# Kernel tuning notes

Hardware: AMD Instinct MI355X
Metric: run time of the kernel (lower is better)

## Reference

```python
import jax, jax.numpy as jnp
import numpy as np
import math

N, NP, D, H, W, HEADS = 4, 1024, 256, 64, 64, 8
DH = D // HEADS


def _norm_coords(height, width):
    # (height*width, 2) with (x, y) in [0, 1], row-major flatten (y outer, x inner)
    y = jnp.linspace(0.0, 1.0, height)
    x = jnp.linspace(0.0, 1.0, width)
    yg, xg = jnp.meshgrid(y, x, indexing='ij')
    return jnp.stack([xg.reshape(-1), yg.reshape(-1)], axis=-1)


def _pos_enc(coords, dim):
    # coords: (P, 2) -> (P, dim); even slots sin(x*div), odd slots cos(y*div)
    div = jnp.exp(jnp.arange(0, dim, 2, dtype=coords.dtype) * (-math.log(10000.0) / dim))
    s = jnp.sin(coords[:, 0:1] * div)  # (P, dim/2)
    c = jnp.cos(coords[:, 1:2] * div)  # (P, dim/2)
    return jnp.stack([s, c], axis=-1).reshape(coords.shape[0], dim)


def setup_inputs() -> dict:
    key = jax.random.key(0)
    ks = jax.random.split(key, 10)
    sc = 1.0 / math.sqrt(D)
    return {
        "local_feat": jax.random.normal(ks[0], (N, NP, D), jnp.float32),
        "global_feat": jax.random.normal(ks[1], (N, D, H, W), jnp.float32),
        "Wq": jax.random.normal(ks[2], (D, D), jnp.float32) * sc,
        "bq": jax.random.normal(ks[3], (D,), jnp.float32) * sc,
        "Wk": jax.random.normal(ks[4], (D, D), jnp.float32) * sc,
        "bk": jax.random.normal(ks[5], (D,), jnp.float32) * sc,
        "Wv": jax.random.normal(ks[6], (D, D), jnp.float32) * sc,
        "bv": jax.random.normal(ks[7], (D,), jnp.float32) * sc,
        "Wo": jax.random.normal(ks[8], (D, D), jnp.float32) * sc,
        "bo": jax.random.normal(ks[9], (D,), jnp.float32) * sc,
    }


def reference(local_feat, global_feat, Wq, bq, Wk, bk, Wv, bv, Wo, bo):
    n, N_p, d = local_feat.shape
    _, _, h, w = global_feat.shape
    hw = h * w
    P = int(math.sqrt(N_p))

    gf = jnp.transpose(global_feat.reshape(n, d, hw), (0, 2, 1))  # (n, HW, d)

    lf = local_feat + _pos_enc(_norm_coords(P, P), d)[None]       # (n, N_p, d)
    gf = gf + _pos_enc(_norm_coords(h, w), d)[None]               # (n, HW, d)

    q = (lf @ Wq.T + bq).reshape(n, N_p, HEADS, DH)
    k = (gf @ Wk.T + bk).reshape(n, hw, HEADS, DH)
    v = (gf @ Wv.T + bv).reshape(n, hw, HEADS, DH)

    scores = jnp.einsum('bqhd,bkhd->bhqk', q, k) / math.sqrt(DH)  # (n, H, N_p, HW)
    attn = jax.nn.softmax(scores, axis=-1)
    out = jnp.einsum('bhqk,bkhd->bqhd', attn, v).reshape(n, N_p, d)

    return (lf + out) @ Wo.T + bo
```

## Files before the change

### kernel.cpp

```cpp
#include <hip/hip_runtime.h>
#include <hip/hip_bf16.h>
#include <math.h>

#define NB    4
#define NPTS  1024
#define DD    256
#define HWW   4096
#define NHEAD 8
#define DHD   32
#define VTROW 4128

typedef short s8v  __attribute__((ext_vector_type(8)));
typedef float f4v  __attribute__((ext_vector_type(4)));
typedef unsigned int u2v __attribute__((ext_vector_type(2)));
typedef unsigned int u4v __attribute__((ext_vector_type(4)));

#define MFMA_BF16 __builtin_amdgcn_mfma_f32_16x16x32_bf16

#define PE_FACT (-9.210340371976184f / 256.0f)
#define QSCALE 0.2550348637f

#if defined(__has_builtin)
#if __has_builtin(__builtin_amdgcn_permlane16_swap) && __has_builtin(__builtin_amdgcn_permlane32_swap)
#define HAVE_PLSWAP 1
#endif
#endif

__device__ __forceinline__ unsigned packbf(float hi, float lo) {
    return __builtin_amdgcn_perm(__float_as_uint(hi), __float_as_uint(lo), 0x07060302u);
}

__device__ __forceinline__ void swap2(unsigned a, unsigned b, unsigned& x, unsigned& y) {
#ifdef HAVE_PLSWAP
    u2v r1 = __builtin_amdgcn_permlane32_swap(a, b, false, false);
    u2v r2 = __builtin_amdgcn_permlane16_swap(r1.x, r1.y, false, false);
    x = r2.x; y = r2.y;
#else
    int l = threadIdx.x & 63;
    int i0 = ((((l >> 4) & 1) << 5) | (l & 15)) << 2;
    unsigned pa = (unsigned)__builtin_amdgcn_ds_bpermute(i0, (int)a);
    unsigned pb = (unsigned)__builtin_amdgcn_ds_bpermute(i0, (int)b);
    x = (l < 32) ? pa : pb;
    unsigned qa = (unsigned)__builtin_amdgcn_ds_bpermute(i0 + 64, (int)a);
    unsigned qb = (unsigned)__builtin_amdgcn_ds_bpermute(i0 + 64, (int)b);
    y = (l < 32) ? qa : qb;
#endif
}

__global__ __launch_bounds__(256) void prep_local(const float* __restrict__ lf,
                                                  __hip_bfloat16* __restrict__ lf_pe_b) {
    int idx = blockIdx.x * 256 + threadIdx.x;
    int c = idx & 255;
    int p = (idx >> 8) & 1023;
    float div = __expf((float)(c & ~1) * PE_FACT);
    float pe;
    if (c & 1) {
        float y = (float)(p >> 5) * (1.0f / 31.0f);
        pe = __cosf(y * div);
    } else {
        float x = (float)(p & 31) * (1.0f / 31.0f);
        pe = __sinf(x * div);
    }
    lf_pe_b[idx] = __float2bfloat16(lf[idx] + pe);
}

__global__ __launch_bounds__(1024) void prep_global(const float* __restrict__ gfeat,
                                                    __hip_bfloat16* __restrict__ gf_pe_b) {
    __shared__ float tile[32][33];
    int n  = blockIdx.z;
    int p0 = blockIdx.x * 32;
    int c0 = blockIdx.y * 32;
    int tx = threadIdx.x, ty = threadIdx.y;
    tile[ty][tx] = gfeat[((size_t)n * DD + (c0 + ty)) * HWW + p0 + tx];
    __syncthreads();
    int p = p0 + ty, c = c0 + tx;
    float div = __expf((float)(c & ~1) * PE_FACT);
    float pe;
    if (c & 1) {
        float y = (float)(p >> 6) * (1.0f / 63.0f);
        pe = __cosf(y * div);
    } else {
        float x = (float)(p & 63) * (1.0f / 63.0f);
        pe = __sinf(x * div);
    }
    gf_pe_b[((size_t)n * HWW + p) * DD + c] = __float2bfloat16(tile[tx][ty] + pe);
}

__global__ __launch_bounds__(256) void w2b(const float* __restrict__ wq, const float* __restrict__ wk,
                                           const float* __restrict__ wv, const float* __restrict__ wo,
                                           __hip_bfloat16* __restrict__ out) {
    int idx = blockIdx.x * 256 + threadIdx.x;
    int m = idx >> 16, r = idx & 65535;
    const float* src = (m == 0) ? wq : (m == 1) ? wk : (m == 2) ? wv : wo;
    out[idx] = __float2bfloat16(src[r]);
}

template <int MODE>
__global__ __launch_bounds__(256) void gemm256(const __hip_bfloat16* __restrict__ A,
                                               const __hip_bfloat16* __restrict__ Wb,
                                               const float* __restrict__ bias,
                                               void* __restrict__ outp) {
    int wave = threadIdx.x >> 6;
    int lane = threadIdx.x & 63;
    int quad = lane >> 4, c16 = lane & 15;
    int m0 = blockIdx.x * 64 + wave * 16;
    int c0 = blockIdx.y * 64;
    const short* ap  = (const short*)A + (m0 + c16) * DD + quad * 8;
    const short* wp  = (const short*)Wb + (c0 + c16) * DD + quad * 8;

    f4v acc0 = {0.f, 0.f, 0.f, 0.f}, acc1 = acc0, acc2 = acc0, acc3 = acc0;

    s8v a  = *(const s8v*)(ap);
    s8v b0 = *(const s8v*)(wp);
    s8v b1 = *(const s8v*)(wp + 16 * DD);
    s8v b2 = *(const s8v*)(wp + 32 * DD);
    s8v b3 = *(const s8v*)(wp + 48 * DD);
#pragma unroll
    for (int ks = 0; ks < 8; ++ks) {
        s8v an, bn0, bn1, bn2, bn3;
        if (ks < 7) {
            int o = (ks + 1) * 32;
            an  = *(const s8v*)(ap + o);
            bn0 = *(const s8v*)(wp + o);
            bn1 = *(const s8v*)(wp + o + 16 * DD);
            bn2 = *(const s8v*)(wp + o + 32 * DD);
            bn3 = *(const s8v*)(wp + o + 48 * DD);
        }
        acc0 = MFMA_BF16(a, b0, acc0, 0, 0, 0);
        acc1 = MFMA_BF16(a, b1, acc1, 0, 0, 0);
        acc2 = MFMA_BF16(a, b2, acc2, 0, 0, 0);
        acc3 = MFMA_BF16(a, b3, acc3, 0, 0, 0);
        if (ks < 7) { a = an; b0 = bn0; b1 = bn1; b2 = bn2; b3 = bn3; }
    }
#pragma unroll
    for (int t = 0; t < 4; ++t) {
        f4v acc = (t == 0) ? acc0 : (t == 1) ? acc1 : (t == 2) ? acc2 : acc3;
        int col = c0 + t * 16 + c16;
        float bv = bias[col];
#pragma unroll
        for (int r = 0; r < 4; ++r) {
            int row = m0 + quad * 4 + r;
            float v = acc[r] + bv;
            if (MODE == 0) {
                int n = row >> 10, p = row & 1023, h = col >> 5, dh = col & 31;
                ((__hip_bfloat16*)outp)[(((size_t)(n * NHEAD + h) << 10) + p) * DHD + dh] =
                    __float2bfloat16(v * QSCALE);
            } else {
                ((float*)outp)[(size_t)row * DD + col] = v;
            }
        }
    }
}

__global__ __launch_bounds__(256) void gemmKV(const __hip_bfloat16* __restrict__ A,
                                              const __hip_bfloat16* __restrict__ Wk,
                                              const __hip_bfloat16* __restrict__ Wv,
                                              const float* __restrict__ bk,
                                              const float* __restrict__ bv,
                                              __hip_bfloat16* __restrict__ Kb,
                                              __hip_bfloat16* __restrict__ Vtb) {
    __shared__ __align__(16) unsigned stv[64][36];

    int tid = threadIdx.x;
    int wave = tid >> 6;
    int lane = tid & 63;
    int quad = lane >> 4, c16 = lane & 15;
    int m0 = blockIdx.x * 64 + wave * 16;
    int c0 = blockIdx.y * 64;
    const short* ap  = (const short*)A + (m0 + c16) * DD + quad * 8;
    const short* wkp = (const short*)Wk + (c0 + c16) * DD + quad * 8;
    const short* wvp = (const short*)Wv + (c0 + c16) * DD + quad * 8;

    f4v ak0 = {0.f,0.f,0.f,0.f}, ak1 = ak0, ak2 = ak0, ak3 = ak0;
    f4v av0 = ak0, av1 = ak0, av2 = ak0, av3 = ak0;

    s8v a  = *(const s8v*)(ap);
    s8v k0 = *(const s8v*)(wkp);
    s8v k1 = *(const s8v*)(wkp + 16 * DD);
    s8v k2 = *(const s8v*)(wkp + 32 * DD);
    s8v k3 = *(const s8v*)(wkp + 48 * DD);
    s8v v0 = *(const s8v*)(wvp);
    s8v v1 = *(const s8v*)(wvp + 16 * DD);
    s8v v2 = *(const s8v*)(wvp + 32 * DD);
    s8v v3 = *(const s8v*)(wvp + 48 * DD);
#pragma unroll
    for (int ks = 0; ks < 8; ++ks) {
        s8v an, kn0, kn1, kn2, kn3, vn0, vn1, vn2, vn3;
        if (ks < 7) {
            int o = (ks + 1) * 32;
            an  = *(const s8v*)(ap + o);
            kn0 = *(const s8v*)(wkp + o);
            kn1 = *(const s8v*)(wkp + o + 16 * DD);
            kn2 = *(const s8v*)(wkp + o + 32 * DD);
            kn3 = *(const s8v*)(wkp + o + 48 * DD);
            vn0 = *(const s8v*)(wvp + o);
            vn1 = *(const s8v*)(wvp + o + 16 * DD);
            vn2 = *(const s8v*)(wvp + o + 32 * DD);
            vn3 = *(const s8v*)(wvp + o + 48 * DD);
        }
        ak0 = MFMA_BF16(a, k0, ak0, 0, 0, 0);
        ak1 = MFMA_BF16(a, k1, ak1, 0, 0, 0);
        ak2 = MFMA_BF16(a, k2, ak2, 0, 0, 0);
        ak3 = MFMA_BF16(a, k3, ak3, 0, 0, 0);
        av0 = MFMA_BF16(a, v0, av0, 0, 0, 0);
        av1 = MFMA_BF16(a, v1, av1, 0, 0, 0);
        av2 = MFMA_BF16(a, v2, av2, 0, 0, 0);
        av3 = MFMA_BF16(a, v3, av3, 0, 0, 0);
        if (ks < 7) {
            a = an; k0 = kn0; k1 = kn1; k2 = kn2; k3 = kn3;
            v0 = vn0; v1 = vn1; v2 = vn2; v3 = vn3;
        }
    }
    int nblk = (blockIdx.x * 64) >> 12;
    int kb   = (blockIdx.x * 64) & 4095;
#pragma unroll
    for (int t = 0; t < 4; ++t) {
        f4v accK = (t == 0) ? ak0 : (t == 1) ? ak1 : (t == 2) ? ak2 : ak3;
        f4v accV = (t == 0) ? av0 : (t == 1) ? av1 : (t == 2) ? av2 : av3;
        int col = c0 + t * 16 + c16;
        float bkv = bk[col], bvv = bv[col];
        int h = col >> 5, dh = col & 31;
#pragma unroll
        for (int r = 0; r < 4; ++r) {
            int row = m0 + quad * 4 + r;
            int p = row & 4095;
            Kb[(((size_t)(nblk * NHEAD + h) << 12) + p) * DHD + dh] = __float2bfloat16(accK[r] + bkv);
        }
#pragma unroll
        for (int rp = 0; rp < 2; ++rp) {
            __hip_bfloat16 lo = __float2bfloat16(accV[2 * rp] + bvv);
            __hip_bfloat16 hi = __float2bfloat16(accV[2 * rp + 1] + bvv);
            unsigned dw = (unsigned)*(unsigned short*)&lo | ((unsigned)*(unsigned short*)&hi << 16);
            stv[t * 16 + c16][wave * 8 + quad * 2 + rp] = dw;
        }
    }
    __syncthreads();
    int col = tid >> 2;
    int kd  = (tid & 3) * 8;
    u4v w0 = *(const u4v*)&stv[col][kd];
    u4v w1 = *(const u4v*)&stv[col][kd + 4];
    int gh  = (c0 + col) >> 5, gdh = (c0 + col) & 31;
    short* vp = (short*)Vtb + ((size_t)(nblk * NHEAD + gh) * DHD + gdh) * VTROW + kb + kd * 2;
    *(u4v*)(vp)     = w0;
    *(u4v*)(vp + 8) = w1;
}

template <int NC>
__global__ __launch_bounds__(256) void attn(const __hip_bfloat16* __restrict__ Q,
                                            const __hip_bfloat16* __restrict__ Kg,
                                            const __hip_bfloat16* __restrict__ Vt,
                                            __hip_bfloat16* __restrict__ Opart,
                                            float* __restrict__ lpart) {
    constexpr int CK = HWW / NC;
    constexpr int NSTEP = CK / 32;

    int tid = threadIdx.x;
    int wave = tid >> 6, lane = tid & 63;
    int quad = lane >> 4, c16 = lane & 15;

    int id = blockIdx.x;
    int xcd = id & 7;
    int s = id >> 3;
    int qtile = s & 3;
    int gidx = ((s >> 2) << 3) | xcd;
    int bh = gidx & 31;
    int chunk = gidx >> 5;

    int q0 = qtile * 256 + wave * 64;

    const short* Qs = (const short*)Q + (size_t)bh * NPTS * DHD;
    const short* Ks = (const short*)Kg + ((size_t)bh * HWW + (size_t)chunk * CK) * DHD;
    const short* Vs = (const short*)Vt + (size_t)bh * DHD * VTROW + (size_t)chunk * CK;

    s8v aq[4];
#pragma unroll
    for (int g = 0; g < 4; ++g)
        aq[g] = *(const s8v*)(Qs + (q0 + g * 16 + c16) * DHD + quad * 8);

    const f4v zf = {0.f, 0.f, 0.f, 0.f};
    f4v o[4][2];
#pragma unroll
    for (int g = 0; g < 4; ++g) { o[g][0] = zf; o[g][1] = zf; }
    float lsum[4] = {0.f, 0.f, 0.f, 0.f};

    const short* kbase  = Ks + c16 * DHD + quad * 8;
    const short* v0base = Vs + c16 * VTROW + quad * 8;
    const short* v1base = Vs + (16 + c16) * VTROW + quad * 8;

    s8v kfA = *(const s8v*)(kbase);
    s8v kfB = *(const s8v*)(kbase + 16 * DHD);
    s8v vfA = *(const s8v*)(v0base);
    s8v vfB = *(const s8v*)(v1base);

    for (int st = 0; st < NSTEP; ++st) {
        bool more = (st + 1) < NSTEP;
        s8v nkA, nkB, nvA, nvB;
        if (more) {
            int ko = (st + 1) * 32;
            nkA = *(const s8v*)(kbase + ko * DHD);
            nkB = *(const s8v*)(kbase + ko * DHD + 16 * DHD);
            nvA = *(const s8v*)(v0base + ko);
            nvB = *(const s8v*)(v1base + ko);
        }
#pragma unroll
        for (int g = 0; g < 4; ++g) {
            f4v sA = MFMA_BF16(kfA, aq[g], zf, 0, 0, 0);
            f4v sB = MFMA_BF16(kfB, aq[g], zf, 0, 0, 0);
            float pA0 = __builtin_amdgcn_exp2f(sA[0]);
            float pA1 = __builtin_amdgcn_exp2f(sA[1]);
            float pA2 = __builtin_amdgcn_exp2f(sA[2]);
            float pA3 = __builtin_amdgcn_exp2f(sA[3]);
            float pB0 = __builtin_amdgcn_exp2f(sB[0]);
            float pB1 = __builtin_amdgcn_exp2f(sB[1]);
            float pB2 = __builtin_amdgcn_exp2f(sB[2]);
            float pB3 = __builtin_amdgcn_exp2f(sB[3]);
            lsum[g] += ((pA0 + pA1) + (pA2 + pA3)) + ((pB0 + pB1) + (pB2 + pB3));
            unsigned a0 = packbf(pA1, pA0);
            unsigned a1 = packbf(pA3, pA2);
            unsigned b0 = packbf(pB1, pB0);
            unsigned b1 = packbf(pB3, pB2);
            unsigned x0, y0, x1, y1;
            swap2(a0, b0, x0, y0);
            swap2(a1, b1, x1, y1);
            union { u4v u; s8v s; } pf;
            pf.u = (u4v){x0, x1, y0, y1};
            o[g][0] = MFMA_BF16(vfA, pf.s, o[g][0], 0, 0, 0);
            o[g][1] = MFMA_BF16(vfB, pf.s, o[g][1], 0, 0, 0);
        }
        if (more) { kfA = nkA; kfB = nkB; vfA = nvA; vfB = nvB; }
    }

    size_t obase = (size_t)(chunk * 32 + bh) * NPTS;
#pragma unroll
    for (int g = 0; g < 4; ++g) {
        float l = lsum[g];
        l += __shfl_xor(l, 16);
        l += __shfl_xor(l, 32);
        int q = q0 + g * 16 + c16;
        if (quad == 0) lpart[obase + q] = l;
        unsigned d0 = packbf(o[g][0][1], o[g][0][0]);
        unsigned d1 = packbf(o[g][0][3], o[g][0][2]);
        unsigned d2 = packbf(o[g][1][1], o[g][1][0]);
        unsigned d3 = packbf(o[g][1][3], o[g][1][2]);
        unsigned* op = (unsigned*)Opart + (obase + q) * (DHD / 2);
        *(u2v*)(op + 2 * quad)     = (u2v){d0, d1};
        *(u2v*)(op + 8 + 2 * quad) = (u2v){d2, d3};
    }
}

template <int NC>
__global__ __launch_bounds__(256) void combine(const __hip_bfloat16* __restrict__ Opart,
                                               const float* __restrict__ lpart,
                                               const __hip_bfloat16* __restrict__ lf_pe,
                                               __hip_bfloat16* __restrict__ outb) {
    int idx = blockIdx.x * 256 + threadIdx.x;
    int c = idx & 255;
    int q = (idx >> 8) & 1023;
    int n = idx >> 18;
    int h = c >> 5, dh = c & 31;
    size_t bhq = ((size_t)(n * NHEAD + h) << 10) + q;
    float l = 0.f, o = 0.f;
#pragma unroll
    for (int ch = 0; ch < NC; ++ch) {
        l += lpart[(size_t)ch * 32 * NPTS + bhq];
        o += __bfloat162float(Opart[((size_t)ch * 32 * NPTS + bhq) * DHD + dh]);
    }
    outb[idx] = __float2bfloat16(o / l + __bfloat162float(lf_pe[idx]));
}

extern "C" void kernel_launch(void* const* d_in, const int* in_sizes, int n_in,
                              void* d_out, int out_size, void* d_ws, size_t ws_size,
                              hipStream_t stream) {
    const float* lf    = (const float*)d_in[0];
    const float* gfeat = (const float*)d_in[1];
    const float* Wq    = (const float*)d_in[2];
    const float* bq    = (const float*)d_in[3];
    const float* Wk    = (const float*)d_in[4];
    const float* bk    = (const float*)d_in[5];
    const float* Wv    = (const float*)d_in[6];
    const float* bv    = (const float*)d_in[7];
    const float* Wo    = (const float*)d_in[8];
    const float* bo    = (const float*)d_in[9];

    const size_t MB = 1u << 20;
    char* ws = (char*)d_ws;
    __hip_bfloat16* lf_pe_b = (__hip_bfloat16*)(ws);
    __hip_bfloat16* gf_pe_b = (__hip_bfloat16*)(ws + 2 * MB);
    __hip_bfloat16* W4      = (__hip_bfloat16*)(ws + 10 * MB);
    __hip_bfloat16* Qb      = (__hip_bfloat16*)(ws + 10 * MB + 512 * 1024);
    __hip_bfloat16* Kb      = (__hip_bfloat16*)(ws + 12 * MB + 512 * 1024);
    __hip_bfloat16* Vtb     = (__hip_bfloat16*)(ws + 20 * MB + 512 * 1024);
    __hip_bfloat16* ALb     = (__hip_bfloat16*)(ws + 29 * MB);
    float*          lpart   = (float*)(ws + 31 * MB);
    __hip_bfloat16* Opart   = (__hip_bfloat16*)(ws + 32 * MB);

    prep_local<<<dim3(NB * NPTS * DD / 256), dim3(256), 0, stream>>>(lf, lf_pe_b);
    prep_global<<<dim3(HWW / 32, DD / 32, NB), dim3(32, 32), 0, stream>>>(gfeat, gf_pe_b);
    w2b<<<dim3(4 * DD * DD / 256), dim3(256), 0, stream>>>(Wq, Wk, Wv, Wo, W4);

    gemm256<0><<<dim3(NB * NPTS / 64, 4), dim3(256), 0, stream>>>(lf_pe_b, W4, bq, (void*)Qb);
    gemmKV<<<dim3(NB * HWW / 64, 4), dim3(256), 0, stream>>>(gf_pe_b, W4 + 1 * DD * DD,
                                                             W4 + 2 * DD * DD, bk, bv, Kb, Vtb);

    if (ws_size >= 48 * MB) {
        attn<8><<<dim3(128 * 8), dim3(256), 0, stream>>>(Qb, Kb, Vtb, Opart, lpart);
        combine<8><<<dim3(NB * NPTS * DD / 256), dim3(256), 0, stream>>>(Opart, lpart, lf_pe_b, ALb);
    } else if (ws_size >= 40 * MB) {
        attn<4><<<dim3(128 * 4), dim3(256), 0, stream>>>(Qb, Kb, Vtb, Opart, lpart);
        combine<4><<<dim3(NB * NPTS * DD / 256), dim3(256), 0, stream>>>(Opart, lpart, lf_pe_b, ALb);
    } else if (ws_size >= 36 * MB) {
        attn<2><<<dim3(128 * 2), dim3(256), 0, stream>>>(Qb, Kb, Vtb, Opart, lpart);
        combine<2><<<dim3(NB * NPTS * DD / 256), dim3(256), 0, stream>>>(Opart, lpart, lf_pe_b, ALb);
    } else {
        attn<1><<<dim3(128 * 1), dim3(256), 0, stream>>>(Qb, Kb, Vtb, Opart, lpart);
        combine<1><<<dim3(NB * NPTS * DD / 256), dim3(256), 0, stream>>>(Opart, lpart, lf_pe_b, ALb);
    }

    gemm256<3><<<dim3(NB * NPTS / 64, 4), dim3(256), 0, stream>>>(ALb, W4 + 3 * DD * DD, bo, d_out);
}
```

Baseline: 182.4 us.

## Merge prep and projection kernels, fuse combine with output GEMM, drop permlane swaps

```diff
diff --git a/kernel.cpp b/kernel.cpp
--- a/kernel.cpp
+++ b/kernel.cpp
@@ -20,229 +20,176 @@
 #define PE_FACT (-9.210340371976184f / 256.0f)
 #define QSCALE 0.2550348637f
 
-#if defined(__has_builtin)
-#if __has_builtin(__builtin_amdgcn_permlane16_swap) && __has_builtin(__builtin_amdgcn_permlane32_swap)
-#define HAVE_PLSWAP 1
-#endif
-#endif
-
 __device__ __forceinline__ unsigned packbf(float hi, float lo) {
     return __builtin_amdgcn_perm(__float_as_uint(hi), __float_as_uint(lo), 0x07060302u);
 }
 
-__device__ __forceinline__ void swap2(unsigned a, unsigned b, unsigned& x, unsigned& y) {
-#ifdef HAVE_PLSWAP
-    u2v r1 = __builtin_amdgcn_permlane32_swap(a, b, false, false);
-    u2v r2 = __builtin_amdgcn_permlane16_swap(r1.x, r1.y, false, false);
-    x = r2.x; y = r2.y;
-#else
-    int l = threadIdx.x & 63;
-    int i0 = ((((l >> 4) & 1) << 5) | (l & 15)) << 2;
-    unsigned pa = (unsigned)__builtin_amdgcn_ds_bpermute(i0, (int)a);
-    unsigned pb = (unsigned)__builtin_amdgcn_ds_bpermute(i0, (int)b);
-    x = (l < 32) ? pa : pb;
-    unsigned qa = (unsigned)__builtin_amdgcn_ds_bpermute(i0 + 64, (int)a);
-    unsigned qb = (unsigned)__builtin_amdgcn_ds_bpermute(i0 + 64, (int)b);
-    y = (l < 32) ? qa : qb;
-#endif
-}
-
-__global__ __launch_bounds__(256) void prep_local(const float* __restrict__ lf,
-                                                  __hip_bfloat16* __restrict__ lf_pe_b) {
-    int idx = blockIdx.x * 256 + threadIdx.x;
-    int c = idx & 255;
-    int p = (idx >> 8) & 1023;
-    float div = __expf((float)(c & ~1) * PE_FACT);
-    float pe;
-    if (c & 1) {
-        float y = (float)(p >> 5) * (1.0f / 31.0f);
-        pe = __cosf(y * div);
+__global__ __launch_bounds__(256) void prep(const float* __restrict__ lf,
+                                            const float* __restrict__ gfeat,
+                                            const float* __restrict__ wq,
+                                            const float* __restrict__ wk,
+                                            const float* __restrict__ wv,
+                                            const float* __restrict__ wo,
+                                            __hip_bfloat16* __restrict__ lf_pe_b,
+                                            __hip_bfloat16* __restrict__ gf_pe_b,
+                                            __hip_bfloat16* __restrict__ W4) {
+    __shared__ float tile[32][33];
+    int b = blockIdx.x, tid = threadIdx.x;
+    if (b < 4096) {
+        int idx = b * 256 + tid;
+        int c = idx & 255, p = (idx >> 8) & 1023;
+        float div = __expf((float)(c & ~1) * PE_FACT);
+        float pe = (c & 1) ? __cosf((float)(p >> 5) * (1.0f / 31.0f) * div)
+                           : __sinf((float)(p & 31) * (1.0f / 31.0f) * div);
+        lf_pe_b[idx] = __float2bfloat16(lf[idx] + pe);
+    } else if (b < 8192) {
+        int t = b - 4096;
+        int n = t >> 10, r = t & 1023;
+        int p0 = (r >> 3) * 32, c0 = (r & 7) * 32;
+        int tx = tid & 31, ty = tid >> 5;
+#pragma unroll
+        for (int i = 0; i < 4; ++i)
+            tile[ty + 8 * i][tx] = gfeat[((size_t)n * DD + (c0 + ty + 8 * i)) * HWW + p0 + tx];
+        __syncthreads();
+#pragma unroll
+        for (int i = 0; i < 4; ++i) {
+            int p = p0 + ty + 8 * i, c = c0 + tx;
+            float div = __expf((float)(c & ~1) * PE_FACT);
+            float pe = (c & 1) ? __cosf((float)(p >> 6) * (1.0f / 63.0f) * div)
+                               : __sinf((float)(p & 63) * (1.0f / 63.0f) * div);
+            gf_pe_b[((size_t)n * HWW + p) * DD + c] = __float2bfloat16(tile[tx][ty + 8 * i] + pe);
+        }
     } else {
-        float x = (float)(p & 31) * (1.0f / 31.0f);
-        pe = __sinf(x * div);
-    }
-    lf_pe_b[idx] = __float2bfloat16(lf[idx] + pe);
-}
-
-__global__ __launch_bounds__(1024) void prep_global(const float* __restrict__ gfeat,
-                                                    __hip_bfloat16* __restrict__ gf_pe_b) {
-    __shared__ float tile[32][33];
-    int n  = blockIdx.z;
-    int p0 = blockIdx.x * 32;
-    int c0 = blockIdx.y * 32;
-    int tx = threadIdx.x, ty = threadIdx.y;
-    tile[ty][tx] = gfeat[((size_t)n * DD + (c0 + ty)) * HWW + p0 + tx];
-    __syncthreads();
-    int p = p0 + ty, c = c0 + tx;
-    float div = __expf((float)(c & ~1) * PE_FACT);
-    float pe;
-    if (c & 1) {
-        float y = (float)(p >> 6) * (1.0f / 63.0f);
-        pe = __cosf(y * div);
+        int idx = (b - 8192) * 256 + tid;
+        int m = idx >> 16, r = idx & 65535;
+        const float* src = (m == 0) ? wq : (m == 1) ? wk : (m == 2) ? wv : wo;
+        W4[idx] = __float2bfloat16(src[r]);
+    }
+}
+
+__global__ __launch_bounds__(256) void gemmQKV(const __hip_bfloat16* __restrict__ Aq,
+                                               const __hip_bfloat16* __restrict__ Akv,
+                                               const __hip_bfloat16* __restrict__ W4,
+                                               const float* __restrict__ bq,
+                                               const float* __restrict__ bk,
+                                               const float* __restrict__ bv,
+                                               __hip_bfloat16* __restrict__ Qb,
+                                               __hip_bfloat16* __restrict__ Kb,
+                                               __hip_bfloat16* __restrict__ Vtb) {
+    __shared__ __align__(16) unsigned stv[64][36];
+    int tid = threadIdx.x;
+    int wave = tid >> 6, lane = tid & 63;
+    int quad = lane >> 4, c16 = lane & 15;
+    int b = blockIdx.x;
+
+    if (b < 256) {
+        int m0 = (b & 63) * 64 + wave * 16;
+        int c0 = (b >> 6) * 64;
+        const short* ap = (const short*)Aq + (m0 + c16) * DD + quad * 8;
+        const short* wp = (const short*)W4 + (c0 + c16) * DD + quad * 8;
+        f4v acc0 = {0.f,0.f,0.f,0.f}, acc1 = acc0, acc2 = acc0, acc3 = acc0;
+#pragma unroll
+        for (int ks = 0; ks < 8; ++ks) {
+            int o = ks * 32;
+            s8v a  = *(const s8v*)(ap + o);
+            s8v b0 = *(const s8v*)(wp + o);
+            s8v b1 = *(const s8v*)(wp + o + 16 * DD);
+            s8v b2 = *(const s8v*)(wp + o + 32 * DD);
+            s8v b3 = *(const s8v*)(wp + o + 48 * DD);
+            acc0 = MFMA_BF16(a, b0, acc0, 0, 0, 0);
+            acc1 = MFMA_BF16(a, b1, acc1, 0, 0, 0);
+            acc2 = MFMA_BF16(a, b2, acc2, 0, 0, 0);
+            acc3 = MFMA_BF16(a, b3, acc3, 0, 0, 0);
+        }
+#pragma unroll
+        for (int t = 0; t < 4; ++t) {
+            f4v acc = (t == 0) ? acc0 : (t == 1) ? acc1 : (t == 2) ? acc2 : acc3;
+            int col = c0 + t * 16 + c16;
+            float bvv = bq[col];
+            int h = col >> 5, dh = col & 31;
+#pragma unroll
+            for (int r = 0; r < 4; ++r) {
+                int row = m0 + quad * 4 + r;
+                int n = row >> 10, p = row & 1023;
+                Qb[(((size_t)(n * NHEAD + h) << 10) + p) * DHD + dh] =
+                    __float2bfloat16((acc[r] + bvv) * QSCALE);
+            }
+        }
     } else {
-        float x = (float)(p & 63) * (1.0f / 63.0f);
-        pe = __sinf(x * div);
-    }
-    gf_pe_b[((size_t)n * HWW + p) * DD + c] = __float2bfloat16(tile[tx][ty] + pe);
-}
-
-__global__ __launch_bounds__(256) void w2b(const float* __restrict__ wq, const float* __restrict__ wk,
-                                           const float* __restrict__ wv, const float* __restrict__ wo,
-                                           __hip_bfloat16* __restrict__ out) {
-    int idx = blockIdx.x * 256 + threadIdx.x;
-    int m = idx >> 16, r = idx & 65535;
-    const float* src = (m == 0) ? wq : (m == 1) ? wk : (m == 2) ? wv : wo;
-    out[idx] = __float2bfloat16(src[r]);
-}
-
-template <int MODE>
-__global__ __launch_bounds__(256) void gemm256(const __hip_bfloat16* __restrict__ A,
-                                               const __hip_bfloat16* __restrict__ Wb,
-                                               const float* __restrict__ bias,
-                                               void* __restrict__ outp) {
-    int wave = threadIdx.x >> 6;
-    int lane = threadIdx.x & 63;
-    int quad = lane >> 4, c16 = lane & 15;
-    int m0 = blockIdx.x * 64 + wave * 16;
-    int c0 = blockIdx.y * 64;
-    const short* ap  = (const short*)A + (m0 + c16) * DD + quad * 8;
-    const short* wp  = (const short*)Wb + (c0 + c16) * DD + quad * 8;
-
-    f4v acc0 = {0.f, 0.f, 0.f, 0.f}, acc1 = acc0, acc2 = acc0, acc3 = acc0;
-
-    s8v a  = *(const s8v*)(ap);
-    s8v b0 = *(const s8v*)(wp);
-    s8v b1 = *(const s8v*)(wp + 16 * DD);
-    s8v b2 = *(const s8v*)(wp + 32 * DD);
-    s8v b3 = *(const s8v*)(wp + 48 * DD);
-#pragma unroll
-    for (int ks = 0; ks < 8; ++ks) {
-        s8v an, bn0, bn1, bn2, bn3;
-        if (ks < 7) {
-            int o = (ks + 1) * 32;
-            an  = *(const s8v*)(ap + o);
-            bn0 = *(const s8v*)(wp + o);
-            bn1 = *(const s8v*)(wp + o + 16 * DD);
-            bn2 = *(const s8v*)(wp + o + 32 * DD);
-            bn3 = *(const s8v*)(wp + o + 48 * DD);
-        }
-        acc0 = MFMA_BF16(a, b0, acc0, 0, 0, 0);
-        acc1 = MFMA_BF16(a, b1, acc1, 0, 0, 0);
-        acc2 = MFMA_BF16(a, b2, acc2, 0, 0, 0);
-        acc3 = MFMA_BF16(a, b3, acc3, 0, 0, 0);
-        if (ks < 7) { a = an; b0 = bn0; b1 = bn1; b2 = bn2; b3 = bn3; }
-    }
-#pragma unroll
-    for (int t = 0; t < 4; ++t) {
-        f4v acc = (t == 0) ? acc0 : (t == 1) ? acc1 : (t == 2) ? acc2 : acc3;
-        int col = c0 + t * 16 + c16;
-        float bv = bias[col];
-#pragma unroll
-        for (int r = 0; r < 4; ++r) {
-            int row = m0 + quad * 4 + r;
-            float v = acc[r] + bv;
-            if (MODE == 0) {
-                int n = row >> 10, p = row & 1023, h = col >> 5, dh = col & 31;
-                ((__hip_bfloat16*)outp)[(((size_t)(n * NHEAD + h) << 10) + p) * DHD + dh] =
-                    __float2bfloat16(v * QSCALE);
-            } else {
-                ((float*)outp)[(size_t)row * DD + col] = v;
+        int b2 = b - 256;
+        int mblk = b2 & 255;
+        int m0 = mblk * 64 + wave * 16;
+        int c0 = (b2 >> 8) * 64;
+        const short* ap  = (const short*)Akv + (m0 + c16) * DD + quad * 8;
+        const short* wkp = (const short*)W4 + DD * DD     + (c0 + c16) * DD + quad * 8;
+        const short* wvp = (const short*)W4 + 2 * DD * DD + (c0 + c16) * DD + quad * 8;
+        f4v ak0 = {0.f,0.f,0.f,0.f}, ak1 = ak0, ak2 = ak0, ak3 = ak0;
+        f4v av0 = ak0, av1 = ak0, av2 = ak0, av3 = ak0;
+#pragma unroll
+        for (int ks = 0; ks < 8; ++ks) {
+            int o = ks * 32;
+            s8v a  = *(const s8v*)(ap + o);
+            s8v k0 = *(const s8v*)(wkp + o);
+            s8v k1 = *(const s8v*)(wkp + o + 16 * DD);
+            s8v k2 = *(const s8v*)(wkp + o + 32 * DD);
+            s8v k3 = *(const s8v*)(wkp + o + 48 * DD);
+            ak0 = MFMA_BF16(a, k0, ak0, 0, 0, 0);
+            ak1 = MFMA_BF16(a, k1, ak1, 0, 0, 0);
+            ak2 = MFMA_BF16(a, k2, ak2, 0, 0, 0);
+            ak3 = MFMA_BF16(a, k3, ak3, 0, 0, 0);
+            s8v v0 = *(const s8v*)(wvp + o);
+            s8v v1 = *(const s8v*)(wvp + o + 16 * DD);
+            s8v v2 = *(const s8v*)(wvp + o + 32 * DD);
+            s8v v3 = *(const s8v*)(wvp + o + 48 * DD);
+            av0 = MFMA_BF16(a, v0, av0, 0, 0, 0);
+            av1 = MFMA_BF16(a, v1, av1, 0, 0, 0);
+            av2 = MFMA_BF16(a, v2, av2, 0, 0, 0);
+            av3 = MFMA_BF16(a, v3, av3, 0, 0, 0);
+        }
+        int blkbase = mblk * 64;
+        int nblk = blkbase >> 12;
+        int kb   = blkbase & 4095;
+#pragma unroll
+        for (int t = 0; t < 4; ++t) {
+            f4v accK = (t == 0) ? ak0 : (t == 1) ? ak1 : (t == 2) ? ak2 : ak3;
+            f4v accV = (t == 0) ? av0 : (t == 1) ? av1 : (t == 2) ? av2 : av3;
+            int col = c0 + t * 16 + c16;
+            float bkv = bk[col], bvv = bv[col];
+            int h = col >> 5, dh = col & 31;
+#pragma unroll
+            for (int r = 0; r < 4; ++r) {
+                int row = m0 + quad * 4 + r;
+                int p = row & 4095;
+                Kb[(((size_t)(nblk * NHEAD + h) << 12) + p) * DHD + dh] =
+                    __float2bfloat16(accK[r] + bkv);
             }
-        }
-    }
-}
-
-__global__ __launch_bounds__(256) void gemmKV(const __hip_bfloat16* __restrict__ A,
-                                              const __hip_bfloat16* __restrict__ Wk,
-                                              const __hip_bfloat16* __restrict__ Wv,
-                                              const float* __restrict__ bk,
-                                              const float* __restrict__ bv,
-                                              __hip_bfloat16* __restrict__ Kb,
-                                              __hip_bfloat16* __restrict__ Vtb) {
-    __shared__ __align__(16) unsigned stv[64][36];
-
-    int tid = threadIdx.x;
-    int wave = tid >> 6;
-    int lane = tid & 63;
-    int quad = lane >> 4, c16 = lane & 15;
-    int m0 = blockIdx.x * 64 + wave * 16;
-    int c0 = blockIdx.y * 64;
-    const short* ap  = (const short*)A + (m0 + c16) * DD + quad * 8;
-    const short* wkp = (const short*)Wk + (c0 + c16) * DD + quad * 8;
-    const short* wvp = (const short*)Wv + (c0 + c16) * DD + quad * 8;
-
-    f4v ak0 = {0.f,0.f,0.f,0.f}, ak1 = ak0, ak2 = ak0, ak3 = ak0;
-    f4v av0 = ak0, av1 = ak0, av2 = ak0, av3 = ak0;
-
-    s8v a  = *(const s8v*)(ap);
-    s8v k0 = *(const s8v*)(wkp);
-    s8v k1 = *(const s8v*)(wkp + 16 * DD);
-    s8v k2 = *(const s8v*)(wkp + 32 * DD);
-    s8v k3 = *(const s8v*)(wkp + 48 * DD);
-    s8v v0 = *(const s8v*)(wvp);
-    s8v v1 = *(const s8v*)(wvp + 16 * DD);
-    s8v v2 = *(const s8v*)(wvp + 32 * DD);
-    s8v v3 = *(const s8v*)(wvp + 48 * DD);
-#pragma unroll
-    for (int ks = 0; ks < 8; ++ks) {
-        s8v an, kn0, kn1, kn2, kn3, vn0, vn1, vn2, vn3;
-        if (ks < 7) {
-            int o = (ks + 1) * 32;
-            an  = *(const s8v*)(ap + o);
-            kn0 = *(const s8v*)(wkp + o);
-            kn1 = *(const s8v*)(wkp + o + 16 * DD);
-            kn2 = *(const s8v*)(wkp + o + 32 * DD);
-            kn3 = *(const s8v*)(wkp + o + 48 * DD);
-            vn0 = *(const s8v*)(wvp + o);
-            vn1 = *(const s8v*)(wvp + o + 16 * DD);
-            vn2 = *(const s8v*)(wvp + o + 32 * DD);
-            vn3 = *(const s8v*)(wvp + o + 48 * DD);
-        }
-        ak0 = MFMA_BF16(a, k0, ak0, 0, 0, 0);
-        ak1 = MFMA_BF16(a, k1, ak1, 0, 0, 0);
-        ak2 = MFMA_BF16(a, k2, ak2, 0, 0, 0);
-        ak3 = MFMA_BF16(a, k3, ak3, 0, 0, 0);
-        av0 = MFMA_BF16(a, v0, av0, 0, 0, 0);
-        av1 = MFMA_BF16(a, v1, av1, 0, 0, 0);
-        av2 = MFMA_BF16(a, v2, av2, 0, 0, 0);
-        av3 = MFMA_BF16(a, v3, av3, 0, 0, 0);
-        if (ks < 7) {
-            a = an; k0 = kn0; k1 = kn1; k2 = kn2; k3 = kn3;
-            v0 = vn0; v1 = vn1; v2 = vn2; v3 = vn3;
-        }
-    }
-    int nblk = (blockIdx.x * 64) >> 12;
-    int kb   = (blockIdx.x * 64) & 4095;
-#pragma unroll
-    for (int t = 0; t < 4; ++t) {
-        f4v accK = (t == 0) ? ak0 : (t == 1) ? ak1 : (t == 2) ? ak2 : ak3;
-        f4v accV = (t == 0) ? av0 : (t == 1) ? av1 : (t == 2) ? av2 : av3;
-        int col = c0 + t * 16 + c16;
-        float bkv = bk[col], bvv = bv[col];
-        int h = col >> 5, dh = col & 31;
-#pragma unroll
-        for (int r = 0; r < 4; ++r) {
-            int row = m0 + quad * 4 + r;
-            int p = row & 4095;
-            Kb[(((size_t)(nblk * NHEAD + h) << 12) + p) * DHD + dh] = __float2bfloat16(accK[r] + bkv);
-        }
-#pragma unroll
-        for (int rp = 0; rp < 2; ++rp) {
-            __hip_bfloat16 lo = __float2bfloat16(accV[2 * rp] + bvv);
-            __hip_bfloat16 hi = __float2bfloat16(accV[2 * rp + 1] + bvv);
-            unsigned dw = (unsigned)*(unsigned short*)&lo | ((unsigned)*(unsigned short*)&hi << 16);
-            stv[t * 16 + c16][wave * 8 + quad * 2 + rp] = dw;
-        }
-    }
-    __syncthreads();
-    int col = tid >> 2;
-    int kd  = (tid & 3) * 8;
-    u4v w0 = *(const u4v*)&stv[col][kd];
-    u4v w1 = *(const u4v*)&stv[col][kd + 4];
-    int gh  = (c0 + col) >> 5, gdh = (c0 + col) & 31;
-    short* vp = (short*)Vtb + ((size_t)(nblk * NHEAD + gh) * DHD + gdh) * VTROW + kb + kd * 2;
-    *(u4v*)(vp)     = w0;
-    *(u4v*)(vp + 8) = w1;
+#pragma unroll
+            for (int rp = 0; rp < 2; ++rp) {
+                __hip_bfloat16 lo = __float2bfloat16(accV[2 * rp] + bvv);
+                __hip_bfloat16 hi = __float2bfloat16(accV[2 * rp + 1] + bvv);
+                unsigned dw = (unsigned)*(unsigned short*)&lo | ((unsigned)*(unsigned short*)&hi << 16);
+                stv[t * 16 + c16][wave * 8 + quad * 2 + rp] = dw;
+            }
+        }
+        __syncthreads();
+        int col = tid >> 2;
+        int kd  = (tid & 3) * 8;
+        int grp = kd & 16;
+        int ob  = kd & 15;
+        unsigned vals[8];
+#pragma unroll
+        for (int i = 0; i < 8; ++i) {
+            int o = ob + i;
+            int idw = ((o >> 2) << 1) | (o & 1) | ((o & 2) << 2);
+            vals[i] = stv[col][grp + idw];
+        }
+        u4v w0 = {vals[0], vals[1], vals[2], vals[3]};
+        u4v w1 = {vals[4], vals[5], vals[6], vals[7]};
+        int gh = (c0 + col) >> 5, gdh = (c0 + col) & 31;
+        short* vp = (short*)Vtb + ((size_t)(nblk * NHEAD + gh) * DHD + gdh) * VTROW + kb + kd * 2;
+        *(u4v*)(vp)     = w0;
+        *(u4v*)(vp + 8) = w1;
+    }
 }
 
 template <int NC>
@@ -315,15 +262,9 @@
             float pB2 = __builtin_amdgcn_exp2f(sB[2]);
             float pB3 = __builtin_amdgcn_exp2f(sB[3]);
             lsum[g] += ((pA0 + pA1) + (pA2 + pA3)) + ((pB0 + pB1) + (pB2 + pB3));
-            unsigned a0 = packbf(pA1, pA0);
-            unsigned a1 = packbf(pA3, pA2);
-            unsigned b0 = packbf(pB1, pB0);
-            unsigned b1 = packbf(pB3, pB2);
-            unsigned x0, y0, x1, y1;
-            swap2(a0, b0, x0, y0);
-            swap2(a1, b1, x1, y1);
             union { u4v u; s8v s; } pf;
-            pf.u = (u4v){x0, x1, y0, y1};
+            pf.u = (u4v){packbf(pA1, pA0), packbf(pA3, pA2),
+                         packbf(pB1, pB0), packbf(pB3, pB2)};
             o[g][0] = MFMA_BF16(vfA, pf.s, o[g][0], 0, 0, 0);
             o[g][1] = MFMA_BF16(vfB, pf.s, o[g][1], 0, 0, 0);
         }
@@ -349,23 +290,76 @@
 }
 
 template <int NC>
-__global__ __launch_bounds__(256) void combine(const __hip_bfloat16* __restrict__ Opart,
-                                               const float* __restrict__ lpart,
-                                               const __hip_bfloat16* __restrict__ lf_pe,
-                                               __hip_bfloat16* __restrict__ outb) {
-    int idx = blockIdx.x * 256 + threadIdx.x;
-    int c = idx & 255;
-    int q = (idx >> 8) & 1023;
-    int n = idx >> 18;
-    int h = c >> 5, dh = c & 31;
-    size_t bhq = ((size_t)(n * NHEAD + h) << 10) + q;
-    float l = 0.f, o = 0.f;
-#pragma unroll
-    for (int ch = 0; ch < NC; ++ch) {
-        l += lpart[(size_t)ch * 32 * NPTS + bhq];
-        o += __bfloat162float(Opart[((size_t)ch * 32 * NPTS + bhq) * DHD + dh]);
-    }
-    outb[idx] = __float2bfloat16(o / l + __bfloat162float(lf_pe[idx]));
+__global__ __launch_bounds__(256) void combineO(const __hip_bfloat16* __restrict__ Opart,
+                                                const float* __restrict__ lpart,
+                                                const __hip_bfloat16* __restrict__ lf_pe,
+                                                const __hip_bfloat16* __restrict__ Wo4,
+                                                const float* __restrict__ bo,
+                                                float* __restrict__ out) {
+    __shared__ __align__(16) short al[32][264];
+    int tid = threadIdx.x;
+    int m0 = blockIdx.x * 32;
+    {
+        int rl = tid >> 3;
+        int h  = tid & 7;
+        int rg = m0 + rl;
+        int n = rg >> 10, q = rg & 1023;
+        size_t bhq = ((size_t)(n * NHEAD + h) << 10) + q;
+        float l = 0.f;
+        float ov[32];
+#pragma unroll
+        for (int d = 0; d < 32; ++d) ov[d] = 0.f;
+#pragma unroll
+        for (int ch = 0; ch < NC; ++ch) {
+            size_t base = (size_t)ch * 32 * NPTS + bhq;
+            l += lpart[base];
+            const unsigned* op = (const unsigned*)((const short*)Opart + base * DHD);
+#pragma unroll
+            for (int dw = 0; dw < 16; ++dw) {
+                unsigned u = op[dw];
+                ov[2 * dw]     += __uint_as_float(u << 16);
+                ov[2 * dw + 1] += __uint_as_float(u & 0xffff0000u);
+            }
+        }
+        float linv = 1.0f / l;
+        const unsigned* lp = (const unsigned*)((const short*)lf_pe + ((size_t)rg * DD + h * 32));
+        unsigned* dst = (unsigned*)&al[rl][h * 32];
+#pragma unroll
+        for (int dw = 0; dw < 16; ++dw) {
+            unsigned u = lp[dw];
+            float x0 = ov[2 * dw] * linv     + __uint_as_float(u << 16);
+            float x1 = ov[2 * dw + 1] * linv + __uint_as_float(u & 0xffff0000u);
+            dst[dw] = packbf(x1, x0);
+        }
+    }
+    __syncthreads();
+    int wave = tid >> 6, lane = tid & 63;
+    int quad = lane >> 4, c16 = lane & 15;
+    int rw  = (wave & 1) * 16;
+    int ch0 = (wave >> 1) * 128;
+    f4v acc[8];
+#pragma unroll
+    for (int t = 0; t < 8; ++t) acc[t] = (f4v){0.f, 0.f, 0.f, 0.f};
+#pragma unroll
+    for (int ks = 0; ks < 8; ++ks) {
+        s8v af = *(const s8v*)&al[rw + c16][ks * 32 + quad * 8];
+#pragma unroll
+        for (int t = 0; t < 8; ++t) {
+            const short* wp = (const short*)Wo4 + (ch0 + t * 16 + c16) * DD + ks * 32 + quad * 8;
+            s8v bf = *(const s8v*)wp;
+            acc[t] = MFMA_BF16(af, bf, acc[t], 0, 0, 0);
+        }
+    }
+#pragma unroll
+    for (int t = 0; t < 8; ++t) {
+        int col = ch0 + t * 16 + c16;
+        float bv = bo[col];
+#pragma unroll
+        for (int r = 0; r < 4; ++r) {
+            int row = m0 + rw + quad * 4 + r;
+            out[(size_t)row * DD + col] = acc[t][r] + bv;
+        }
+    }
 }
 
 extern "C" void kernel_launch(void* const* d_in, const int* in_sizes, int n_in,
@@ -390,31 +384,29 @@
     __hip_bfloat16* Qb      = (__hip_bfloat16*)(ws + 10 * MB + 512 * 1024);
     __hip_bfloat16* Kb      = (__hip_bfloat16*)(ws + 12 * MB + 512 * 1024);
     __hip_bfloat16* Vtb     = (__hip_bfloat16*)(ws + 20 * MB + 512 * 1024);
-    __hip_bfloat16* ALb     = (__hip_bfloat16*)(ws + 29 * MB);
     float*          lpart   = (float*)(ws + 31 * MB);
     __hip_bfloat16* Opart   = (__hip_bfloat16*)(ws + 32 * MB);
 
-    prep_local<<<dim3(NB * NPTS * DD / 256), dim3(256), 0, stream>>>(lf, lf_pe_b);
-    prep_global<<<dim3(HWW / 32, DD / 32, NB), dim3(32, 32), 0, stream>>>(gfeat, gf_pe_b);
-    w2b<<<dim3(4 * DD * DD / 256), dim3(256), 0, stream>>>(Wq, Wk, Wv, Wo, W4);
-
-    gemm256<0><<<dim3(NB * NPTS / 64, 4), dim3(256), 0, stream>>>(lf_pe_b, W4, bq, (void*)Qb);
-    gemmKV<<<dim3(NB * HWW / 64, 4), dim3(256), 0, stream>>>(gf_pe_b, W4 + 1 * DD * DD,
-                                                             W4 + 2 * DD * DD, bk, bv, Kb, Vtb);
+    prep<<<dim3(9216), dim3(256), 0, stream>>>(lf, gfeat, Wq, Wk, Wv, Wo,
+                                               lf_pe_b, gf_pe_b, W4);
+    gemmQKV<<<dim3(1280), dim3(256), 0, stream>>>(lf_pe_b, gf_pe_b, W4, bq, bk, bv,
+                                                  Qb, Kb, Vtb);
 
     if (ws_size >= 48 * MB) {
         attn<8><<<dim3(128 * 8), dim3(256), 0, stream>>>(Qb, Kb, Vtb, Opart, lpart);
-        combine<8><<<dim3(NB * NPTS * DD / 256), dim3(256), 0, stream>>>(Opart, lpart, lf_pe_b, ALb);
+        combineO<8><<<dim3(128), dim3(256), 0, stream>>>(Opart, lpart, lf_pe_b,
+                                                         W4 + 3 * DD * DD, bo, (float*)d_out);
     } else if (ws_size >= 40 * MB) {
         attn<4><<<dim3(128 * 4), dim3(256), 0, stream>>>(Qb, Kb, Vtb, Opart, lpart);
-        combine<4><<<dim3(NB * NPTS * DD / 256), dim3(256), 0, stream>>>(Opart, lpart, lf_pe_b, ALb);
+        combineO<4><<<dim3(128), dim3(256), 0, stream>>>(Opart, lpart, lf_pe_b,
+                                                         W4 + 3 * DD * DD, bo, (float*)d_out);
     } else if (ws_size >= 36 * MB) {
         attn<2><<<dim3(128 * 2), dim3(256), 0, stream>>>(Qb, Kb, Vtb, Opart, lpart);
-        combine<2><<<dim3(NB * NPTS * DD / 256), dim3(256), 0, stream>>>(Opart, lpart, lf_pe_b, ALb);
+        combineO<2><<<dim3(128), dim3(256), 0, stream>>>(Opart, lpart, lf_pe_b,
+                                                         W4 + 3 * DD * DD, bo, (float*)d_out);
     } else {
         attn<1><<<dim3(128 * 1), dim3(256), 0, stream>>>(Qb, Kb, Vtb, Opart, lpart);
-        combine<1><<<dim3(NB * NPTS * DD / 256), dim3(256), 0, stream>>>(Opart, lpart, lf_pe_b, ALb);
-    }
-
-    gemm256<3><<<dim3(NB * NPTS / 64, 4), dim3(256), 0, stream>>>(ALb, W4 + 3 * DD * DD, bo, d_out);
-}
+        combineO<1><<<dim3(128), dim3(256), 0, stream>>>(Opart, lpart, lf_pe_b,
+                                                         W4 + 3 * DD * DD, bo, (float*)d_out);
+    }
+}
```

Result: faster. 177.1 us (-2.9%).
